# Performance work log

Measured on AMD Instinct MI355X. Metric: run time of the kernel, lower is better.

Reference implementation:

```python
import math
import jax, jax.numpy as jnp
from jax import lax
import numpy as np

B, C, H, W = 2, 48, 64, 64
DI, DS, DCONV, DTR = 96, 16, 4, 3   # d_inner=expand*dim, d_state, d_conv, dt_rank=ceil(48/16)
HF = 96                              # SEFN hidden = dim * ffn_expansion_factor(2)


def _posenc(L, d):
    pos = jnp.arange(L, dtype=jnp.float32)[:, None]
    div = jnp.exp(jnp.arange(0, d, 2, dtype=jnp.float32) * (-math.log(10000.0) / d))
    pe = jnp.zeros((L, d), jnp.float32)
    pe = pe.at[:, 0::2].set(jnp.sin(pos * div))
    pe = pe.at[:, 1::2].set(jnp.cos(pos * div))
    return pe


def _ln(x, w, b, eps=1e-5):  # last-dim LayerNorm, biased variance (torch unbiased=False)
    mu = x.mean(-1, keepdims=True)
    var = ((x - mu) ** 2).mean(-1, keepdims=True)
    return (x - mu) / jnp.sqrt(var + eps) * w + b


def _ln4d(x, w, b):  # WithBias LayerNorm over channel dim of NCHW (to_3d/to_4d round trip)
    b_, c_, h_, w_ = x.shape
    xf = x.reshape(b_, c_, h_ * w_).transpose(0, 2, 1)
    return _ln(xf, w, b).transpose(0, 2, 1).reshape(b_, c_, h_, w_)


def _flip_odd(x):  # flip last axis on odd rows of axis -2 (snake reordering)
    return x.at[:, :, 1::2, :].set(x[:, :, 1::2, ::-1])


def _conv2d(x, w, bias=None, groups=1, pad=0):
    y = lax.conv_general_dilated(x, w, (1, 1), [(pad, pad), (pad, pad)],
                                 feature_group_count=groups,
                                 dimension_numbers=('NCHW', 'OIHW', 'NCHW'))
    if bias is not None:
        y = y + bias[None, :, None, None]
    return y


def _mamba(x, inproj, convw, convb, xproj, dtw, dtb, Alog, D, outproj):
    # standard mamba_ssm Mamba forward; x: (B, L, C)
    b_, L, _ = x.shape
    xz = x @ inproj.T                      # (B, L, 2*DI)
    xm, z = xz[..., :DI], xz[..., DI:]
    xc = xm.transpose(0, 2, 1)             # (B, DI, L)
    xc = lax.conv_general_dilated(xc, convw, (1,), [(DCONV - 1, 0)],
                                  feature_group_count=DI,
                                  dimension_numbers=('NCH', 'OIH', 'NCH'))
    xc = jax.nn.silu(xc + convb[None, :, None]).transpose(0, 2, 1)  # (B, L, DI)
    x_dbl = xc @ xproj.T                   # (B, L, DTR + 2*DS)
    dt = jax.nn.softplus(x_dbl[..., :DTR] @ dtw.T + dtb)            # (B, L, DI)
    Bm = x_dbl[..., DTR:DTR + DS]          # (B, L, DS)
    Cm = x_dbl[..., DTR + DS:]             # (B, L, DS)
    A = -jnp.exp(Alog)                     # (DI, DS)
    dA = jnp.exp(dt[..., None] * A)        # (B, L, DI, DS)
    dBx = dt[..., None] * Bm[:, :, None, :] * xc[..., None]

    def step(h, t):
        dA_t, dBx_t, C_t = t
        h = dA_t * h + dBx_t
        return h, jnp.einsum('bds,bs->bd', h, C_t)

    h0 = jnp.zeros((b_, DI, DS), x.dtype)
    _, ys = lax.scan(step, h0, (dA.transpose(1, 0, 2, 3), dBx.transpose(1, 0, 2, 3), Cm.transpose(1, 0, 2)))
    y = ys.transpose(1, 0, 2) + xc * D
    y = y * jax.nn.silu(z)
    return y @ outproj.T


def _forward(x, n1_w, n1_b, n2_w, n2_b, mln1_w, mln1_b, mln2_w, mln2_b,
             m1, m2, f_pin, f_dw, f_fus, f_dwa, f_pout,
             f_c1w, f_c1b, f_ln1_w, f_ln1_b, f_c2w, f_c2b, f_ln2_w, f_ln2_b):
    x_spatial = x
    L = H * W
    pe = _posenc(L, C)
    # --- MambaLayer: bidirectional flip-scan ---
    xn = _ln4d(x, n1_w, n1_b)
    rev1 = _flip_odd(xn)                               # snake order over rows
    rev2 = _flip_odd(xn.transpose(0, 1, 3, 2))         # snake order over cols
    x1_flat = rev1.reshape(B, C, L).transpose(0, 2, 1) + pe
    x2_flat = rev2.reshape(B, C, L).transpose(0, 2, 1) + pe
    y1 = _mamba(_ln(x1_flat, mln1_w, mln1_b), *m1)
    y2 = _mamba(_ln(x2_flat, mln2_w, mln2_b), *m2)
    out1 = _flip_odd(y1.transpose(0, 2, 1).reshape(B, C, H, W))
    out2 = _flip_odd(y2.transpose(0, 2, 1).reshape(B, C, W, H)).transpose(0, 1, 3, 2)
    x = x + out1 + out2
    # --- SEFN ---
    xn2 = _ln4d(x, n2_w, n2_b)
    xp = _conv2d(xn2, f_pin)                           # (B, 2*HF, H, W)
    y = x_spatial.reshape(B, C, H // 2, 2, W // 2, 2).mean((3, 5))   # AvgPool2d(2)
    y = jax.nn.relu(_ln4d(_conv2d(y, f_c1w, f_c1b, pad=1), f_ln1_w, f_ln1_b))
    y = jax.nn.relu(_ln4d(_conv2d(y, f_c2w, f_c2b, pad=1), f_ln2_w, f_ln2_b))
    y = jnp.repeat(jnp.repeat(y, 2, axis=2), 2, axis=3)              # nearest Upsample(2)
    xd = _conv2d(xp, f_dw, groups=2 * HF, pad=1)
    x1, x2 = xd[:, :HF], xd[:, HF:]
    x1 = _conv2d(jnp.concatenate([x1, y], axis=1), f_fus)
    x1 = _conv2d(x1, f_dwa, groups=HF, pad=1)
    ff = _conv2d(jax.nn.gelu(x1, approximate=False) * x2, f_pout)
    return x + ff


def setup_inputs():
    key = jax.random.key(0)
    ks = iter(jax.random.split(key, 64))

    def nrm(shape, s):
        return s * jax.random.normal(next(ks), shape, jnp.float32)

    inp = {}
    inp['x'] = nrm((B, C, H, W), 1.0)
    for nm in ['n1', 'n2', 'mln1', 'mln2', 'f_ln1', 'f_ln2']:
        inp[nm + '_w'] = jnp.ones((C,), jnp.float32)
        inp[nm + '_b'] = jnp.zeros((C,), jnp.float32)
    for p in ['m1', 'm2']:
        inp[p + '_inproj'] = nrm((2 * DI, C), 0.1)
        inp[p + '_convw'] = nrm((DI, 1, DCONV), 0.3)
        inp[p + '_convb'] = jnp.zeros((DI,), jnp.float32)
        inp[p + '_xproj'] = nrm((DTR + 2 * DS, DI), 0.1)
        inp[p + '_dtw'] = nrm((DI, DTR), 0.3)
        u = jax.random.uniform(next(ks), (DI,), jnp.float32)
        inp[p + '_dtb'] = jnp.log(jnp.expm1(0.001 + 0.099 * u))  # mamba dt bias init
        inp[p + '_Alog'] = jnp.log(jnp.tile(jnp.arange(1., DS + 1., dtype=jnp.float32), (DI, 1)))
        inp[p + '_D'] = jnp.ones((DI,), jnp.float32)
        inp[p + '_outproj'] = nrm((C, DI), 0.1)
    inp['f_pin'] = nrm((2 * HF, C, 1, 1), 0.1)
    inp['f_dw'] = nrm((2 * HF, 1, 3, 3), 0.2)
    inp['f_fus'] = nrm((HF, HF + C, 1, 1), 0.08)
    inp['f_dwa'] = nrm((HF, 1, 3, 3), 0.2)
    inp['f_pout'] = nrm((C, HF, 1, 1), 0.1)
    inp['f_c1w'] = nrm((C, C, 3, 3), 0.05)
    inp['f_c1b'] = jnp.zeros((C,), jnp.float32)
    inp['f_c2w'] = nrm((C, C, 3, 3), 0.05)
    inp['f_c2b'] = jnp.zeros((C,), jnp.float32)
    return inp


def reference(x, n1_w, n1_b, n2_w, n2_b, mln1_w, mln1_b, mln2_w, mln2_b,
              m1_inproj, m1_convw, m1_convb, m1_xproj, m1_dtw, m1_dtb, m1_Alog, m1_D, m1_outproj,
              m2_inproj, m2_convw, m2_convb, m2_xproj, m2_dtw, m2_dtb, m2_Alog, m2_D, m2_outproj,
              f_pin, f_dw, f_fus, f_dwa, f_pout,
              f_c1w, f_c1b, f_ln1_w, f_ln1_b, f_c2w, f_c2b, f_ln2_w, f_ln2_b):
    m1 = (m1_inproj, m1_convw, m1_convb, m1_xproj, m1_dtw, m1_dtb, m1_Alog, m1_D, m1_outproj)
    m2 = (m2_inproj, m2_convw, m2_convb, m2_xproj, m2_dtw, m2_dtb, m2_Alog, m2_D, m2_outproj)
    return _forward(x, n1_w, n1_b, n2_w, n2_b, mln1_w, mln1_b, mln2_w, mln2_b,
                    m1, m2, f_pin, f_dw, f_fus, f_dwa, f_pout,
                    f_c1w, f_c1b, f_ln1_w, f_ln1_b, f_c2w, f_c2b, f_ln2_w, f_ln2_b)
```

## Files before the change

### kernel.cpp

```cpp
#include <hip/hip_runtime.h>

#define DEV __device__ __forceinline__

DEV float siluf(float x){ return x / (1.f + __expf(-x)); }
DEV float softplusf(float x){ return fmaxf(x, 0.f) + log1pf(expf(-fabsf(x))); }
DEV float geluf(float x){ return 0.5f * x * (1.f + erff(x * 0.70710678118654752440f)); }

__global__ __launch_bounds__(256) void kA_front(const float* __restrict__ x,
    const float* __restrict__ n1w, const float* __restrict__ n1b,
    const float* __restrict__ mw0, const float* __restrict__ mb0,
    const float* __restrict__ mw1, const float* __restrict__ mb1,
    const float* __restrict__ ip0, const float* __restrict__ ip1,
    float* __restrict__ xmg, float* __restrict__ Vg){
  __shared__ alignas(16) float Vl[48*36];
  __shared__ float Wt[48*97];
  __shared__ float mu_s[32], rs_s[32];
  int bd = blockIdx.x >> 7, tile = blockIdx.x & 127;
  int dir = bd >> 1, b = bd & 1;
  int t0 = tile*32;
  int tid = threadIdx.x;
  const float* ip = dir ? ip1 : ip0;
  const float* mw = dir ? mw1 : mw0;
  const float* mb = dir ? mb1 : mb0;
  for (int i = tid; i < 96*48; i += 256){
    int j = i / 48, c = i % 48;
    Wt[c*97 + j] = ip[i];
  }
  for (int i = tid; i < 48*32; i += 256){
    int c = i >> 5, r = i & 31;
    int t = t0 + r;
    int h, w;
    if (dir == 0){ h = t >> 6; int wp = t & 63; w = (h & 1) ? 63 - wp : wp; }
    else         { w = t >> 6; int hp = t & 63; h = (w & 1) ? 63 - hp : hp; }
    Vl[c*36 + r] = x[(size_t)b*48*4096 + c*4096 + h*64 + w];
  }
  __syncthreads();
  {
    int r = tid >> 3, k = tid & 7;
    float s1 = 0.f, s2 = 0.f;
    #pragma unroll
    for (int cc = 0; cc < 6; cc++){
      float v = Vl[(k*6+cc)*36 + r];
      s1 += v; s2 += v*v;
    }
    s1 += __shfl_xor(s1,1); s2 += __shfl_xor(s2,1);
    s1 += __shfl_xor(s1,2); s2 += __shfl_xor(s2,2);
    s1 += __shfl_xor(s1,4); s2 += __shfl_xor(s2,4);
    if (k == 0){
      float m = s1*(1.f/48.f);
      mu_s[r] = m;
      rs_s[r] = rsqrtf(s2*(1.f/48.f) - m*m + 1e-5f);
    }
  }
  __syncthreads();
  for (int i = tid; i < 32*48; i += 256){
    int r = i / 48, c = i % 48;
    int t = t0 + r;
    float v = Vl[c*36 + r];
    float xn = (v - mu_s[r])*rs_s[r]*n1w[c] + n1b[c];
    float ang = (float)t * __expf(-(float)(c & ~1) * (9.210340371976184f/48.f));
    float pe = (c & 1) ? cosf(ang) : sinf(ang);
    Vl[c*36 + r] = xn + pe;
  }
  __syncthreads();
  {
    int r = tid >> 3, k = tid & 7;
    float s1 = 0.f, s2 = 0.f;
    #pragma unroll
    for (int cc = 0; cc < 6; cc++){
      float v = Vl[(k*6+cc)*36 + r];
      s1 += v; s2 += v*v;
    }
    s1 += __shfl_xor(s1,1); s2 += __shfl_xor(s2,1);
    s1 += __shfl_xor(s1,2); s2 += __shfl_xor(s2,2);
    s1 += __shfl_xor(s1,4); s2 += __shfl_xor(s2,4);
    if (k == 0){
      float m = s1*(1.f/48.f);
      mu_s[r] = m;
      rs_s[r] = rsqrtf(s2*(1.f/48.f) - m*m + 1e-5f);
    }
  }
  __syncthreads();
  for (int i = tid; i < 32*48; i += 256){
    int r = i / 48, c = i % 48;
    float v = Vl[c*36 + r];
    float v2 = (v - mu_s[r])*rs_s[r]*mw[c] + mb[c];
    Vl[c*36 + r] = v2;
    Vg[((size_t)bd*4096 + t0 + r)*48 + c] = v2;
  }
  __syncthreads();
  for (int k = 0; k < 3; k++){
    int i = tid + k*256;
    int j = i % 96, rb = i / 96;
    float a0=0.f, a1=0.f, a2=0.f, a3=0.f;
    #pragma unroll 4
    for (int c = 0; c < 48; c++){
      float wv = Wt[c*97 + j];
      const float4 v4 = *(const float4*)&Vl[c*36 + rb*4];
      a0 += wv*v4.x; a1 += wv*v4.y; a2 += wv*v4.z; a3 += wv*v4.w;
    }
    size_t g = ((size_t)bd*4096 + t0 + rb*4)*96 + j;
    xmg[g] = a0; xmg[g+96] = a1; xmg[g+192] = a2; xmg[g+288] = a3;
  }
}

__global__ __launch_bounds__(384) void kB_convscan(const float* __restrict__ xmg,
    const float* __restrict__ cwp0, const float* __restrict__ cwp1,
    const float* __restrict__ cbp0, const float* __restrict__ cbp1,
    const float* __restrict__ xpp0, const float* __restrict__ xpp1,
    const float* __restrict__ dwp0, const float* __restrict__ dwp1,
    const float* __restrict__ dbp0, const float* __restrict__ dbp1,
    const float* __restrict__ Alog0, const float* __restrict__ Alog1,
    float* __restrict__ xcg, float* __restrict__ dtg,
    float* __restrict__ Bmg, float* __restrict__ Cmg,
    float* __restrict__ P, float* __restrict__ S){
  __shared__ union UB {
    float xml[96*36];
    struct { float xwl[35*96]; float xdbl[35*33]; } p;
  } ub;
  __shared__ float xcl[96*33];
  __shared__ float dtl[96*33];
  __shared__ alignas(16) float Bl[32*16], Cl[32*16];
  __shared__ float cw[96*4], cbv[96], dwl[96*3], dbl[96];
  int bd = blockIdx.x >> 7, tile = blockIdx.x & 127;
  int dir = bd >> 1;
  int t0 = tile*32;
  int tid = threadIdx.x;
  const float* cwp = dir ? cwp1 : cwp0;
  const float* cbp = dir ? cbp1 : cbp0;
  const float* xpp = dir ? xpp1 : xpp0;
  const float* dwp = dir ? dwp1 : dwp0;
  const float* dbp = dir ? dbp1 : dbp0;
  const float* Alog = dir ? Alog1 : Alog0;
  for (int i = tid; i < 35*96; i += 384){
    int tl = i / 96, d = i % 96;
    int t = t0 - 3 + tl;
    ub.xml[d*36 + tl] = (t >= 0) ? xmg[((size_t)bd*4096 + t)*96 + d] : 0.f;
  }
  for (int i = tid; i < 96*4;  i += 384) cw[i] = cwp[i];
  for (int i = tid; i < 96*3;  i += 384) dwl[i] = dwp[i];
  for (int i = tid; i < 96;    i += 384){ cbv[i] = cbp[i]; dbl[i] = dbp[i]; }
  __syncthreads();
  for (int i = tid; i < 96*32; i += 384){
    int d = i >> 5, t = i & 31;
    float acc = cbv[d];
    #pragma unroll
    for (int k = 0; k < 4; k++) acc += cw[d*4+k]*ub.xml[d*36 + t + k];
    xcl[d*33 + t] = siluf(acc);
  }
  __syncthreads();
  for (int i = tid; i < 35*96; i += 384) ub.p.xwl[i] = xpp[i];
  __syncthreads();
  for (int i = tid; i < 35*32; i += 384){
    int j = i / 32, t = i % 32;
    float acc = 0.f;
    #pragma unroll 4
    for (int d = 0; d < 96; d++) acc += xcl[d*33 + t]*ub.p.xwl[j*96 + d];
    ub.p.xdbl[j*33 + t] = acc;
  }
  __syncthreads();
  for (int i = tid; i < 96*32; i += 384){
    int d = i >> 5, t = i & 31;
    float v = dbl[d];
    #pragma unroll
    for (int r = 0; r < 3; r++) v += ub.p.xdbl[r*33 + t]*dwl[d*3 + r];
    dtl[d*33 + t] = softplusf(v);
  }
  for (int i = tid; i < 32*16; i += 384){
    int t = i / 16, s = i % 16;
    Bl[t*16 + s] = ub.p.xdbl[(3+s)*33 + t];
    Cl[t*16 + s] = ub.p.xdbl[(19+s)*33 + t];
  }
  __syncthreads();
  for (int i = tid; i < 32*96; i += 384){
    int t = i / 96, d = i % 96;
    size_t g = ((size_t)bd*4096 + t0 + t)*96 + d;
    xcg[g] = xcl[d*33 + t];
    dtg[g] = dtl[d*33 + t];
  }
  for (int i = tid; i < 32*16; i += 384){
    int t = i / 16, s = i % 16;
    size_t g = ((size_t)bd*4096 + t0 + t)*16 + s;
    Bmg[g] = Bl[t*16 + s];
    Cmg[g] = Cl[t*16 + s];
  }
  {
    int d = tid >> 2, q = tid & 3;
    float A0 = -__expf(Alog[d*16 + q*4 + 0]);
    float A1 = -__expf(Alog[d*16 + q*4 + 1]);
    float A2 = -__expf(Alog[d*16 + q*4 + 2]);
    float A3 = -__expf(Alog[d*16 + q*4 + 3]);
    float h0=0.f,h1=0.f,h2=0.f,h3=0.f, p0=1.f,p1=1.f,p2=1.f,p3=1.f;
    #pragma unroll 4
    for (int t = 0; t < 32; t++){
      float dtd = dtl[d*33 + t];
      float u = dtd * xcl[d*33 + t];
      const float4 b4 = *(const float4*)&Bl[t*16 + q*4];
      float a0 = __expf(dtd*A0), a1 = __expf(dtd*A1), a2 = __expf(dtd*A2), a3 = __expf(dtd*A3);
      h0 = a0*h0 + u*b4.x; p0 *= a0;
      h1 = a1*h1 + u*b4.y; p1 *= a1;
      h2 = a2*h2 + u*b4.z; p2 *= a2;
      h3 = a3*h3 + u*b4.w; p3 *= a3;
    }
    size_t ob = (size_t)blockIdx.x*1536 + d*16 + q*4;
    *(float4*)&P[ob] = make_float4(p0,p1,p2,p3);
    *(float4*)&S[ob] = make_float4(h0,h1,h2,h3);
  }
}

__global__ __launch_bounds__(256) void k4_comb(float* __restrict__ P, const float* __restrict__ S){
  int tid2 = blockIdx.x*256 + threadIdx.x;
  int bd = tid2 / 1536, r = tid2 % 1536;
  size_t idx = (size_t)bd*128*1536 + r;
  const int ST = 1536;
  float pb0,pb1,pb2,pb3,pb4,pb5,pb6,pb7, sb0,sb1,sb2,sb3,sb4,sb5,sb6,sb7;
  pb0=P[idx+0*ST]; sb0=S[idx+0*ST]; pb1=P[idx+1*ST]; sb1=S[idx+1*ST];
  pb2=P[idx+2*ST]; sb2=S[idx+2*ST]; pb3=P[idx+3*ST]; sb3=S[idx+3*ST];
  pb4=P[idx+4*ST]; sb4=S[idx+4*ST]; pb5=P[idx+5*ST]; sb5=S[idx+5*ST];
  pb6=P[idx+6*ST]; sb6=S[idx+6*ST]; pb7=P[idx+7*ST]; sb7=S[idx+7*ST];
  float h = 0.f;
  for (int c0 = 0; c0 < 128; c0 += 8){
    float pn0=0,sn0=0,pn1=0,sn1=0,pn2=0,sn2=0,pn3=0,sn3=0;
    float pn4=0,sn4=0,pn5=0,sn5=0,pn6=0,sn6=0,pn7=0,sn7=0;
    if (c0 + 8 < 128){
      pn0=P[idx+(size_t)(c0+8)*ST];  sn0=S[idx+(size_t)(c0+8)*ST];
      pn1=P[idx+(size_t)(c0+9)*ST];  sn1=S[idx+(size_t)(c0+9)*ST];
      pn2=P[idx+(size_t)(c0+10)*ST]; sn2=S[idx+(size_t)(c0+10)*ST];
      pn3=P[idx+(size_t)(c0+11)*ST]; sn3=S[idx+(size_t)(c0+11)*ST];
      pn4=P[idx+(size_t)(c0+12)*ST]; sn4=S[idx+(size_t)(c0+12)*ST];
      pn5=P[idx+(size_t)(c0+13)*ST]; sn5=S[idx+(size_t)(c0+13)*ST];
      pn6=P[idx+(size_t)(c0+14)*ST]; sn6=S[idx+(size_t)(c0+14)*ST];
      pn7=P[idx+(size_t)(c0+15)*ST]; sn7=S[idx+(size_t)(c0+15)*ST];
    }
    P[idx+(size_t)(c0+0)*ST] = h; h = pb0*h + sb0;
    P[idx+(size_t)(c0+1)*ST] = h; h = pb1*h + sb1;
    P[idx+(size_t)(c0+2)*ST] = h; h = pb2*h + sb2;
    P[idx+(size_t)(c0+3)*ST] = h; h = pb3*h + sb3;
    P[idx+(size_t)(c0+4)*ST] = h; h = pb4*h + sb4;
    P[idx+(size_t)(c0+5)*ST] = h; h = pb5*h + sb5;
    P[idx+(size_t)(c0+6)*ST] = h; h = pb6*h + sb6;
    P[idx+(size_t)(c0+7)*ST] = h; h = pb7*h + sb7;
    pb0=pn0;sb0=sn0;pb1=pn1;sb1=sn1;pb2=pn2;sb2=sn2;pb3=pn3;sb3=sn3;
    pb4=pn4;sb4=sn4;pb5=pn5;sb5=sn5;pb6=pn6;sb6=sn6;pb7=pn7;sb7=sn7;
  }
}

__global__ __launch_bounds__(384) void k5_scan2(const float* __restrict__ dtg,
    const float* __restrict__ xcg, const float* __restrict__ Bmg, const float* __restrict__ Cmg,
    const float* __restrict__ Alog0, const float* __restrict__ Alog1,
    const float* __restrict__ Dp0, const float* __restrict__ Dp1,
    const float* __restrict__ ip0, const float* __restrict__ ip1,
    const float* __restrict__ Vg, const float* __restrict__ Hin, float* __restrict__ yout){
  __shared__ union U5 {
    struct { float dts[32*96]; float xcs[32*96]; } s;
    struct { float Wzt[48*96]; float Vgs[32*48]; } e;
  } u;
  __shared__ alignas(16) float Bl[32*16], Cl[32*16];
  __shared__ float yl[32*96];
  int task = blockIdx.x;
  int bd = task >> 7, ch = task & 127;
  int t0 = ch*32;
  int tid = threadIdx.x;
  const float* ip   = (bd >= 2) ? ip1 : ip0;
  const float* Alog = (bd >= 2) ? Alog1 : Alog0;
  const float* Dp   = (bd >= 2) ? Dp1 : Dp0;
  for (int i = tid; i < 32*96; i += 384){
    int t = i / 96, dd = i % 96;
    size_t g = ((size_t)bd*4096 + t0 + t)*96 + dd;
    u.s.dts[i] = dtg[g];
    u.s.xcs[i] = xcg[g];
  }
  for (int i = tid; i < 32*16; i += 384){
    size_t g = ((size_t)bd*4096 + t0)*16 + i;
    Bl[i] = Bmg[g];
    Cl[i] = Cmg[g];
  }
  __syncthreads();
  {
    int d = tid >> 2, q = tid & 3;
    float A0 = -__expf(Alog[d*16 + q*4 + 0]);
    float A1 = -__expf(Alog[d*16 + q*4 + 1]);
    float A2 = -__expf(Alog[d*16 + q*4 + 2]);
    float A3 = -__expf(Alog[d*16 + q*4 + 3]);
    float Dd = Dp[d];
    const float4 h4 = *(const float4*)&Hin[(size_t)task*1536 + d*16 + q*4];
    float h0 = h4.x, h1 = h4.y, h2 = h4.z, h3 = h4.w;
    for (int t = 0; t < 32; t += 2){
      float dtdA = u.s.dts[t*96 + d];
      float xcvA = u.s.xcs[t*96 + d];
      float dtdB = u.s.dts[(t+1)*96 + d];
      float xcvB = u.s.xcs[(t+1)*96 + d];
      float uA = dtdA * xcvA, uB = dtdB * xcvB;
      const float4 b4A = *(const float4*)&Bl[t*16 + q*4];
      const float4 c4A = *(const float4*)&Cl[t*16 + q*4];
      const float4 b4B = *(const float4*)&Bl[(t+1)*16 + q*4];
      const float4 c4B = *(const float4*)&Cl[(t+1)*16 + q*4];
      float a0 = __expf(dtdA*A0), a1 = __expf(dtdA*A1), a2 = __expf(dtdA*A2), a3 = __expf(dtdA*A3);
      float e0 = __expf(dtdB*A0), e1 = __expf(dtdB*A1), e2 = __expf(dtdB*A2), e3 = __expf(dtdB*A3);
      h0 = a0*h0 + uA*b4A.x;
      h1 = a1*h1 + uA*b4A.y;
      h2 = a2*h2 + uA*b4A.z;
      h3 = a3*h3 + uA*b4A.w;
      float pyA = (h0*c4A.x + h1*c4A.y) + (h2*c4A.z + h3*c4A.w);
      h0 = e0*h0 + uB*b4B.x;
      h1 = e1*h1 + uB*b4B.y;
      h2 = e2*h2 + uB*b4B.z;
      h3 = e3*h3 + uB*b4B.w;
      float pyB = (h0*c4B.x + h1*c4B.y) + (h2*c4B.z + h3*c4B.w);
      pyA += __shfl_xor(pyA, 1);  pyB += __shfl_xor(pyB, 1);
      pyA += __shfl_xor(pyA, 2);  pyB += __shfl_xor(pyB, 2);
      if (q == 0){
        yl[t*96 + d]     = pyA + xcvA*Dd;
        yl[(t+1)*96 + d] = pyB + xcvB*Dd;
      }
    }
  }
  __syncthreads();
  for (int i = tid; i < 96*48; i += 384){
    int j = i % 96, c = i / 96;
    u.e.Wzt[c*96 + j] = ip[(96 + j)*48 + c];
  }
  for (int i = tid; i < 32*48; i += 384){
    int t = i / 48, c = i % 48;
    u.e.Vgs[i] = Vg[((size_t)bd*4096 + t0 + t)*48 + c];
  }
  __syncthreads();
  for (int i = tid; i < 32*96; i += 384){
    int t = i / 96, dd = i % 96;
    float z = 0.f;
    #pragma unroll 4
    for (int c = 0; c < 48; c++) z += u.e.Wzt[c*96 + dd] * u.e.Vgs[t*48 + c];
    size_t g = ((size_t)bd*4096 + t0 + t)*96 + dd;
    yout[g] = yl[i] * siluf(z);
  }
}

__global__ __launch_bounds__(384) void k67_mid(const float* __restrict__ x,
    const float* __restrict__ y1, const float* __restrict__ y2,
    const float* __restrict__ op1, const float* __restrict__ op2,
    const float* __restrict__ nw, const float* __restrict__ nb,
    const float* __restrict__ pin,
    float* __restrict__ xmid, float* __restrict__ xp){
  __shared__ float bufW[192*49];
  __shared__ union UL { float ylds[16*97]; struct { float xl[48*17]; float mu[16]; float rs[16]; } l; } ul;
  int bid = blockIdx.x;
  int b = bid >> 8, h = (bid >> 2) & 63, wq = bid & 3;
  int w0 = wq << 4;
  int tid = threadIdx.x;
  int w = tid & 15, cg = tid >> 4;
  float acc0 = 0.f, acc1 = 0.f;
  for (int pass = 0; pass < 2; pass++){
    __syncthreads();
    const float* op = pass ? op2 : op1;
    const float* y  = pass ? y2  : y1;
    for (int i = tid; i < 48*96; i += 384){
      int c = i / 96, d = i % 96;
      bufW[c*97 + d] = op[i];
    }
    if (pass == 0){
      for (int i = tid; i < 16*96; i += 384){
        int wl_ = i / 96, d = i % 96;
        int wsp = w0 + wl_;
        int wp = (h & 1) ? 63 - wsp : wsp;
        ul.ylds[wl_*97 + d] = y[((size_t)b*4096 + h*64 + wp)*96 + d];
      }
    } else {
      for (int i = tid; i < 16*96; i += 384){
        int wl_ = i / 96, d = i % 96;
        int wsp = w0 + wl_;
        int t = wsp*64 + ((wsp & 1) ? 63 - h : h);
        ul.ylds[wl_*97 + d] = y[((size_t)b*4096 + t)*96 + d];
      }
    }
    __syncthreads();
    #pragma unroll 4
    for (int d = 0; d < 96; d++){
      float yv = ul.ylds[w*97 + d];
      acc0 += yv * bufW[(cg*2+0)*97 + d];
      acc1 += yv * bufW[(cg*2+1)*97 + d];
    }
  }
  __syncthreads();
  {
    int c0 = cg*2;
    size_t idx0 = (((size_t)b*48 + c0)*64 + h)*64 + w0 + w;
    float v0 = x[idx0] + acc0;
    xmid[idx0] = v0;
    ul.l.xl[c0*17 + w] = v0;
    size_t idx1 = idx0 + 4096;
    float v1 = x[idx1] + acc1;
    xmid[idx1] = v1;
    ul.l.xl[(c0+1)*17 + w] = v1;
  }
  for (int i = tid; i < 192*48; i += 384){
    int r = i / 48, c = i % 48;
    bufW[r*49 + c] = pin[i];
  }
  __syncthreads();
  if (tid < 128){
    int r = tid >> 3, k = tid & 7;
    float s1 = 0.f, s2 = 0.f;
    #pragma unroll
    for (int cc = 0; cc < 6; cc++){
      float v = ul.l.xl[(k*6+cc)*17 + r];
      s1 += v; s2 += v*v;
    }
    s1 += __shfl_xor(s1,1); s2 += __shfl_xor(s2,1);
    s1 += __shfl_xor(s1,2); s2 += __shfl_xor(s2,2);
    s1 += __shfl_xor(s1,4); s2 += __shfl_xor(s2,4);
    if (k == 0){
      float m = s1*(1.f/48.f);
      ul.l.mu[r] = m;
      ul.l.rs[r] = rsqrtf(s2*(1.f/48.f) - m*m + 1e-5f);
    }
  }
  __syncthreads();
  for (int i = tid; i < 48*16; i += 384){
    int c = i >> 4, ww = i & 15;
    ul.l.xl[c*17 + ww] = (ul.l.xl[c*17 + ww] - ul.l.mu[ww])*ul.l.rs[ww]*nw[c] + nb[c];
  }
  __syncthreads();
  for (int it = 0; it < 2; it++){
    int i = tid + it*384;
    int ww = i & 15, oq = i >> 4;
    int o0 = oq*4;
    float a0=0,a1=0,a2=0,a3=0;
    #pragma unroll 4
    for (int c = 0; c < 48; c++){
      float xv = ul.l.xl[c*17 + ww];
      a0 += xv*bufW[(o0+0)*49 + c];
      a1 += xv*bufW[(o0+1)*49 + c];
      a2 += xv*bufW[(o0+2)*49 + c];
      a3 += xv*bufW[(o0+3)*49 + c];
    }
    xp[(((size_t)b*192 + o0+0)*64 + h)*64 + w0 + ww] = a0;
    xp[(((size_t)b*192 + o0+1)*64 + h)*64 + w0 + ww] = a1;
    xp[(((size_t)b*192 + o0+2)*64 + h)*64 + w0 + ww] = a2;
    xp[(((size_t)b*192 + o0+3)*64 + h)*64 + w0 + ww] = a3;
  }
}

__global__ __launch_bounds__(384) void k9_conv3(const float* __restrict__ in,
    const float* __restrict__ wgt, const float* __restrict__ bias,
    const float* __restrict__ lnw, const float* __restrict__ lnb,
    float* __restrict__ out, int pooled, int lnin){
  __shared__ float wl[12*48*9];
  __shared__ float sin_[48*3*34];
  __shared__ float mu_i[104], rs_i[104];
  int bid = blockIdx.x;
  int cq = bid & 3, i0 = (bid >> 2) & 31, b = bid >> 7;
  int tid = threadIdx.x;
  for (int i = tid; i < 12*48*9; i += 384) wl[i] = wgt[cq*12*48*9 + i];
  for (int i = tid; i < 48*3*34; i += 384){
    int jx = i % 34, ky = (i/34) % 3, ci = i/102;
    int r = i0 + ky - 1, j = jx - 1;
    float v = 0.f;
    if (r >= 0 && r < 32 && j >= 0 && j < 32){
      if (pooled){
        const float* xb = in + (((size_t)b*48 + ci)*64 + 2*r)*64 + 2*j;
        v = 0.25f*(xb[0] + xb[1] + xb[64] + xb[65]);
      } else {
        v = in[(((size_t)b*48 + ci)*32 + r)*32 + j];
      }
    }
    sin_[i] = v;
  }
  __syncthreads();
  if (lnin){
    if (tid < 102){
      int jx = tid % 34, ky = tid / 34;
      int r = i0 + ky - 1, j = jx - 1;
      if (r >= 0 && r < 32 && j >= 0 && j < 32){
        float s1 = 0.f, s2 = 0.f;
        #pragma unroll 4
        for (int ci = 0; ci < 48; ci++){ float v = sin_[ci*102 + tid]; s1 += v; s2 += v*v; }
        float m = s1*(1.f/48.f);
        mu_i[tid] = m;
        rs_i[tid] = rsqrtf(s2*(1.f/48.f) - m*m + 1e-5f);
      }
    }
    __syncthreads();
    for (int i = tid; i < 48*102; i += 384){
      int ci = i / 102, p = i % 102;
      int jx = p % 34, ky = p / 34;
      int r = i0 + ky - 1, j = jx - 1;
      if (r >= 0 && r < 32 && j >= 0 && j < 32){
        float v = (sin_[i] - mu_i[p])*rs_i[p]*lnw[ci] + lnb[ci];
        sin_[i] = fmaxf(v, 0.f);
      }
    }
    __syncthreads();
  }
  int j = tid & 31, col = tid >> 5;
  float acc = bias[cq*12 + col];
  for (int ci = 0; ci < 48; ci++){
    const float* wp = wl + ((size_t)col*48 + ci)*9;
    const float* sp = sin_ + ci*102;
    #pragma unroll
    for (int ky = 0; ky < 3; ky++)
      #pragma unroll
      for (int kx = 0; kx < 3; kx++)
        acc += sp[ky*34 + j + kx] * wp[ky*3 + kx];
  }
  out[(((size_t)b*48 + cq*12 + col)*32 + i0)*32 + j] = acc;
}

__global__ __launch_bounds__(256) void k13_dw(const float* __restrict__ in,
    const float* __restrict__ wgt, float* __restrict__ out, int CH){
  int idx = blockIdx.x*256 + threadIdx.x;
  if (idx >= 2*CH*1024) return;
  int wq = idx & 15, h = (idx >> 4) & 63, c = (idx >> 10) % CH, b = idx / (CH*1024);
  int w0 = wq*4;
  const float* ip = in + ((size_t)b*CH + c)*4096;
  const float* wp = wgt + c*9;
  float a0=0.f,a1=0.f,a2=0.f,a3=0.f;
  #pragma unroll
  for (int ky = 0; ky < 3; ky++){
    int hh = h + ky - 1;
    if (hh < 0 || hh > 63) continue;
    const float* rp = ip + hh*64;
    float v0 = (w0 > 0)  ? rp[w0-1] : 0.f;
    float v1 = rp[w0+0], v2 = rp[w0+1], v3 = rp[w0+2], v4 = rp[w0+3];
    float v5 = (w0 < 60) ? rp[w0+4] : 0.f;
    float k0 = wp[ky*3+0], k1 = wp[ky*3+1], k2 = wp[ky*3+2];
    a0 += k0*v0 + k1*v1 + k2*v2;
    a1 += k0*v1 + k1*v2 + k2*v3;
    a2 += k0*v2 + k1*v3 + k2*v4;
    a3 += k0*v3 + k1*v4 + k2*v5;
  }
  float* op = out + (((size_t)b*CH + c)*64 + h)*64 + w0;
  op[0]=a0; op[1]=a1; op[2]=a2; op[3]=a3;
}

__global__ __launch_bounds__(256) void k14_fus(const float* __restrict__ xd,
    const float* __restrict__ cv2, const float* __restrict__ lnw, const float* __restrict__ lnb,
    const float* __restrict__ fus, float* __restrict__ x1){
  __shared__ float wl[48*144];
  __shared__ float al[96][64];
  __shared__ float yl[48][32];
  __shared__ float muy[32], rsy[32];
  int bid = blockIdx.x;
  int oh = bid & 1, h = (bid >> 1) & 63, b = bid >> 7;
  int tid = threadIdx.x;
  for (int i = tid; i < 48*144; i += 256) wl[i] = fus[(size_t)oh*48*144 + i];
  for (int i = tid; i < 96*64; i += 256){
    int ci = i >> 6, w = i & 63;
    al[ci][w] = xd[(((size_t)b*192 + ci)*64 + h)*64 + w];
  }
  for (int i = tid; i < 48*32; i += 256){
    int cj = i >> 5, j = i & 31;
    yl[cj][j] = cv2[(((size_t)b*48 + cj)*32 + (h >> 1))*32 + j];
  }
  __syncthreads();
  if (tid < 32){
    float s1 = 0.f, s2 = 0.f;
    #pragma unroll 4
    for (int cj = 0; cj < 48; cj++){ float v = yl[cj][tid]; s1 += v; s2 += v*v; }
    float m = s1*(1.f/48.f);
    muy[tid] = m;
    rsy[tid] = rsqrtf(s2*(1.f/48.f) - m*m + 1e-5f);
  }
  __syncthreads();
  for (int i = tid; i < 48*32; i += 256){
    int cj = i >> 5, j = i & 31;
    yl[cj][j] = fmaxf((yl[cj][j] - muy[j])*rsy[j]*lnw[cj] + lnb[cj], 0.f);
  }
  __syncthreads();
  for (int it = 0; it < 3; it++){
    int i = tid + it*256;
    int w = i & 63, ob = i >> 6; int o0 = ob*4;
    float a[4] = {0,0,0,0};
    #pragma unroll 4
    for (int ci = 0; ci < 96; ci++){
      float xv = al[ci][w];
      #pragma unroll
      for (int q = 0; q < 4; q++) a[q] += xv * wl[(o0+q)*144 + ci];
    }
    int w2 = w >> 1;
    #pragma unroll 4
    for (int cj = 0; cj < 48; cj++){
      float yv = yl[cj][w2];
      #pragma unroll
      for (int q = 0; q < 4; q++) a[q] += yv * wl[(o0+q)*144 + 96 + cj];
    }
    #pragma unroll
    for (int q = 0; q < 4; q++)
      x1[(((size_t)b*96 + oh*48 + o0 + q)*64 + h)*64 + w] = a[q];
  }
}

__global__ __launch_bounds__(384) void k16_out(const float* __restrict__ x1,
    const float* __restrict__ xd, const float* __restrict__ dww,
    const float* __restrict__ pout, const float* __restrict__ xmid, float* __restrict__ out){
  __shared__ float wl[48*97];
  __shared__ float xs[96*54];
  __shared__ float gl[96*17];
  __shared__ float dwl[96*9];
  int bid = blockIdx.x;
  int b = bid >> 8, h = (bid >> 2) & 63, wq = bid & 3;
  int w0 = wq << 4;
  int tid = threadIdx.x;
  for (int i = tid; i < 48*96; i += 384){
    int r = i / 96, c = i % 96;
    wl[r*97 + c] = pout[i];
  }
  for (int i = tid; i < 96*9; i += 384) dwl[i] = dww[i];
  for (int i = tid; i < 96*54; i += 384){
    int jx = i % 18, ky = (i/18) % 3, ch = i/54;
    int hh = h + ky - 1, ww_ = w0 + jx - 1;
    float v = 0.f;
    if (hh >= 0 && hh < 64 && ww_ >= 0 && ww_ < 64)
      v = x1[(((size_t)b*96 + ch)*64 + hh)*64 + ww_];
    xs[i] = v;
  }
  __syncthreads();
  for (int i = tid; i < 96*16; i += 384){
    int ch = i >> 4, ww = i & 15;
    const float* wp = dwl + ch*9;
    const float* sp = xs + ch*54;
    float a = 0.f;
    #pragma unroll
    for (int ky = 0; ky < 3; ky++)
      #pragma unroll
      for (int kx = 0; kx < 3; kx++)
        a += sp[ky*18 + ww + kx] * wp[ky*3 + kx];
    float x2 = xd[(((size_t)b*192 + 96 + ch)*64 + h)*64 + w0 + ww];
    gl[ch*17 + ww] = geluf(a) * x2;
  }
  __syncthreads();
  int ww = tid & 15, cg = tid >> 4;
  float a0=0.f, a1=0.f;
  #pragma unroll 4
  for (int ch = 0; ch < 96; ch++){
    float gv = gl[ch*17 + ww];
    a0 += gv * wl[(cg*2+0)*97 + ch];
    a1 += gv * wl[(cg*2+1)*97 + ch];
  }
  {
    int c0 = cg*2;
    size_t idx0 = (((size_t)b*48 + c0)*64 + h)*64 + w0 + ww;
    out[idx0] = xmid[idx0] + a0;
    size_t idx1 = idx0 + 4096;
    out[idx1] = xmid[idx1] + a1;
  }
}

extern "C" void kernel_launch(void* const* d_in, const int* in_sizes, int n_in,
                              void* d_out, int out_size, void* d_ws, size_t ws_size,
                              hipStream_t stream){
  (void)in_sizes; (void)n_in; (void)out_size; (void)ws_size;
  const float* x    = (const float*)d_in[0];
  const float* n1w  = (const float*)d_in[1];
  const float* n1b  = (const float*)d_in[2];
  const float* n2w  = (const float*)d_in[3];
  const float* n2b  = (const float*)d_in[4];
  const float* mlnw[2] = {(const float*)d_in[5], (const float*)d_in[7]};
  const float* mlnb[2] = {(const float*)d_in[6], (const float*)d_in[8]};
  const float* fln1w = (const float*)d_in[9];
  const float* fln1b = (const float*)d_in[10];
  const float* fln2w = (const float*)d_in[11];
  const float* fln2b = (const float*)d_in[12];
  const float* inproj[2]  = {(const float*)d_in[13], (const float*)d_in[22]};
  const float* convw[2]   = {(const float*)d_in[14], (const float*)d_in[23]};
  const float* convb[2]   = {(const float*)d_in[15], (const float*)d_in[24]};
  const float* xproj[2]   = {(const float*)d_in[16], (const float*)d_in[25]};
  const float* dtw[2]     = {(const float*)d_in[17], (const float*)d_in[26]};
  const float* dtbp[2]    = {(const float*)d_in[18], (const float*)d_in[27]};
  const float* Alog[2]    = {(const float*)d_in[19], (const float*)d_in[28]};
  const float* Dp[2]      = {(const float*)d_in[20], (const float*)d_in[29]};
  const float* outproj[2] = {(const float*)d_in[21], (const float*)d_in[30]};
  const float* fpin  = (const float*)d_in[31];
  const float* fdw   = (const float*)d_in[32];
  const float* ffus  = (const float*)d_in[33];
  const float* fdwa  = (const float*)d_in[34];
  const float* fpout = (const float*)d_in[35];
  const float* fc1w  = (const float*)d_in[36];
  const float* fc1b  = (const float*)d_in[37];
  const float* fc2w  = (const float*)d_in[38];
  const float* fc2b  = (const float*)d_in[39];

  float* ws = (float*)d_ws;
  float* xmg = ws + 0;
  float* Vgb = ws + 1572864;
  float* xcg = ws + 2359296;
  float* dtg = ws + 3932160;
  float* Bmg = ws + 5505024;
  float* Cmg = ws + 5767168;
  float* Pb  = ws + 6029312;
  float* Sb  = ws + 6815744;
  float* xmid= ws + 7602176;
  float* yall = xmg;
  float* Hin  = Pb;
  float* ta   = Sb;
  float* tbuf = Sb + 98304;
  float* xpb  = xcg;
  float* xdb  = dtg;
  float* x1b  = Pb;

  kA_front<<<512,256,0,stream>>>(x, n1w, n1b,
      mlnw[0], mlnb[0], mlnw[1], mlnb[1], inproj[0], inproj[1], xmg, Vgb);
  kB_convscan<<<512,384,0,stream>>>(xmg,
      convw[0], convw[1], convb[0], convb[1], xproj[0], xproj[1],
      dtw[0], dtw[1], dtbp[0], dtbp[1], Alog[0], Alog[1],
      xcg, dtg, Bmg, Cmg, Pb, Sb);
  k4_comb  <<<24,256,0,stream>>>(Pb, Sb);
  k5_scan2 <<<512,384,0,stream>>>(dtg, xcg, Bmg, Cmg, Alog[0], Alog[1],
      Dp[0], Dp[1], inproj[0], inproj[1], Vgb, Hin, yall);
  k67_mid  <<<512,384,0,stream>>>(x, yall, yall + 786432, outproj[0], outproj[1],
      n2w, n2b, fpin, xmid, xpb);
  k9_conv3 <<<256,384,0,stream>>>(x,  fc1w, fc1b, fln1w, fln1b, ta,   1, 0);
  k9_conv3 <<<256,384,0,stream>>>(ta, fc2w, fc2b, fln1w, fln1b, tbuf, 0, 1);
  k13_dw   <<<1536,256,0,stream>>>(xpb, fdw, xdb, 192);
  k14_fus  <<<256,256,0,stream>>>(xdb, tbuf, fln2w, fln2b, ffus, x1b);
  k16_out  <<<512,384,0,stream>>>(x1b, xdb, fdwa, fpout, xmid, (float*)d_out);
}
```

Measured before the change: 184.8 us.

## Fuse depthwise 3x3 conv into fusion and output kernels, drop k13_dw

Removes the standalone depthwise conv kernel over 192 channels. The first 96 channels are now convolved inside k14_fus from a halo tile of xp, with k14_fus retiled to 16-wide column chunks over 1024 blocks. The second 96 channels are recomputed inside k16_out alongside the existing depthwise conv. This eliminates one launch and the write and read of the intermediate xd buffer, at the cost of redundant halo loads, extra shared memory, and a reworked 1x1 matmul tiling in k14.

```diff
diff --git a/kernel.cpp b/kernel.cpp
--- a/kernel.cpp
+++ b/kernel.cpp
@@ -505,97 +505,87 @@
   out[(((size_t)b*48 + cq*12 + col)*32 + i0)*32 + j] = acc;
 }
 
-__global__ __launch_bounds__(256) void k13_dw(const float* __restrict__ in,
-    const float* __restrict__ wgt, float* __restrict__ out, int CH){
-  int idx = blockIdx.x*256 + threadIdx.x;
-  if (idx >= 2*CH*1024) return;
-  int wq = idx & 15, h = (idx >> 4) & 63, c = (idx >> 10) % CH, b = idx / (CH*1024);
-  int w0 = wq*4;
-  const float* ip = in + ((size_t)b*CH + c)*4096;
-  const float* wp = wgt + c*9;
-  float a0=0.f,a1=0.f,a2=0.f,a3=0.f;
-  #pragma unroll
-  for (int ky = 0; ky < 3; ky++){
-    int hh = h + ky - 1;
-    if (hh < 0 || hh > 63) continue;
-    const float* rp = ip + hh*64;
-    float v0 = (w0 > 0)  ? rp[w0-1] : 0.f;
-    float v1 = rp[w0+0], v2 = rp[w0+1], v3 = rp[w0+2], v4 = rp[w0+3];
-    float v5 = (w0 < 60) ? rp[w0+4] : 0.f;
-    float k0 = wp[ky*3+0], k1 = wp[ky*3+1], k2 = wp[ky*3+2];
-    a0 += k0*v0 + k1*v1 + k2*v2;
-    a1 += k0*v1 + k1*v2 + k2*v3;
-    a2 += k0*v2 + k1*v3 + k2*v4;
-    a3 += k0*v3 + k1*v4 + k2*v5;
-  }
-  float* op = out + (((size_t)b*CH + c)*64 + h)*64 + w0;
-  op[0]=a0; op[1]=a1; op[2]=a2; op[3]=a3;
-}
-
-__global__ __launch_bounds__(256) void k14_fus(const float* __restrict__ xd,
+__global__ __launch_bounds__(256) void k14_fus(const float* __restrict__ xp,
     const float* __restrict__ cv2, const float* __restrict__ lnw, const float* __restrict__ lnb,
-    const float* __restrict__ fus, float* __restrict__ x1){
-  __shared__ float wl[48*144];
-  __shared__ float al[96][64];
-  __shared__ float yl[48][32];
-  __shared__ float muy[32], rsy[32];
+    const float* __restrict__ dww, const float* __restrict__ fus, float* __restrict__ x1){
+  __shared__ float wl[48*145];
+  __shared__ float xps[96*54];
+  __shared__ float dwl[96*9];
+  __shared__ float ylq[48*9];
+  __shared__ float gl[96*17];
+  __shared__ float muy[8], rsy[8];
   int bid = blockIdx.x;
-  int oh = bid & 1, h = (bid >> 1) & 63, b = bid >> 7;
+  int wq = bid & 3, h = (bid >> 2) & 63, oh = (bid >> 8) & 1, b = bid >> 9;
+  int w0 = wq << 4;
   int tid = threadIdx.x;
-  for (int i = tid; i < 48*144; i += 256) wl[i] = fus[(size_t)oh*48*144 + i];
-  for (int i = tid; i < 96*64; i += 256){
-    int ci = i >> 6, w = i & 63;
-    al[ci][w] = xd[(((size_t)b*192 + ci)*64 + h)*64 + w];
-  }
-  for (int i = tid; i < 48*32; i += 256){
-    int cj = i >> 5, j = i & 31;
-    yl[cj][j] = cv2[(((size_t)b*48 + cj)*32 + (h >> 1))*32 + j];
-  }
-  __syncthreads();
-  if (tid < 32){
+  for (int i = tid; i < 48*144; i += 256){
+    int r = i / 144, c = i % 144;
+    wl[r*145 + c] = fus[(size_t)oh*48*144 + i];
+  }
+  for (int i = tid; i < 96*9; i += 256) dwl[i] = dww[i];
+  for (int i = tid; i < 96*54; i += 256){
+    int jx = i % 18, ky = (i/18) % 3, ci = i/54;
+    int hh = h + ky - 1, ww_ = w0 + jx - 1;
+    float v = 0.f;
+    if (hh >= 0 && hh < 64 && ww_ >= 0 && ww_ < 64)
+      v = xp[(((size_t)b*192 + ci)*64 + hh)*64 + ww_];
+    xps[i] = v;
+  }
+  {
+    int hp = h >> 1, j0 = w0 >> 1;
+    for (int i = tid; i < 48*8; i += 256){
+      int cj = i >> 3, jl = i & 7;
+      ylq[cj*9 + jl] = cv2[(((size_t)b*48 + cj)*32 + hp)*32 + j0 + jl];
+    }
+  }
+  __syncthreads();
+  if (tid < 8){
     float s1 = 0.f, s2 = 0.f;
     #pragma unroll 4
-    for (int cj = 0; cj < 48; cj++){ float v = yl[cj][tid]; s1 += v; s2 += v*v; }
+    for (int cj = 0; cj < 48; cj++){ float v = ylq[cj*9 + tid]; s1 += v; s2 += v*v; }
     float m = s1*(1.f/48.f);
     muy[tid] = m;
     rsy[tid] = rsqrtf(s2*(1.f/48.f) - m*m + 1e-5f);
   }
-  __syncthreads();
-  for (int i = tid; i < 48*32; i += 256){
-    int cj = i >> 5, j = i & 31;
-    yl[cj][j] = fmaxf((yl[cj][j] - muy[j])*rsy[j]*lnw[cj] + lnb[cj], 0.f);
+  for (int i = tid; i < 96*16; i += 256){
+    int ci = i >> 4, ww = i & 15;
+    const float* wp = dwl + ci*9;
+    const float* sp = xps + ci*54;
+    float a = 0.f;
+    #pragma unroll
+    for (int ky = 0; ky < 3; ky++)
+      #pragma unroll
+      for (int kx = 0; kx < 3; kx++)
+        a += sp[ky*18 + ww + kx] * wp[ky*3 + kx];
+    gl[ci*17 + ww] = a;
+  }
+  __syncthreads();
+  for (int i = tid; i < 48*8; i += 256){
+    int cj = i >> 3, jl = i & 7;
+    ylq[cj*9 + jl] = fmaxf((ylq[cj*9 + jl] - muy[jl])*rsy[jl]*lnw[cj] + lnb[cj], 0.f);
   }
   __syncthreads();
   for (int it = 0; it < 3; it++){
     int i = tid + it*256;
-    int w = i & 63, ob = i >> 6; int o0 = ob*4;
-    float a[4] = {0,0,0,0};
-    #pragma unroll 4
-    for (int ci = 0; ci < 96; ci++){
-      float xv = al[ci][w];
-      #pragma unroll
-      for (int q = 0; q < 4; q++) a[q] += xv * wl[(o0+q)*144 + ci];
-    }
-    int w2 = w >> 1;
-    #pragma unroll 4
-    for (int cj = 0; cj < 48; cj++){
-      float yv = yl[cj][w2];
-      #pragma unroll
-      for (int q = 0; q < 4; q++) a[q] += yv * wl[(o0+q)*144 + 96 + cj];
-    }
-    #pragma unroll
-    for (int q = 0; q < 4; q++)
-      x1[(((size_t)b*96 + oh*48 + o0 + q)*64 + h)*64 + w] = a[q];
+    int ww = i & 15, o = i >> 4;
+    float a = 0.f;
+    #pragma unroll 4
+    for (int ci = 0; ci < 96; ci++) a += gl[ci*17 + ww] * wl[o*145 + ci];
+    int jl = ww >> 1;
+    #pragma unroll 4
+    for (int cj = 0; cj < 48; cj++) a += ylq[cj*9 + jl] * wl[o*145 + 96 + cj];
+    x1[(((size_t)b*96 + oh*48 + o)*64 + h)*64 + w0 + ww] = a;
   }
 }
 
 __global__ __launch_bounds__(384) void k16_out(const float* __restrict__ x1,
-    const float* __restrict__ xd, const float* __restrict__ dww,
+    const float* __restrict__ xp, const float* __restrict__ dwa, const float* __restrict__ dwf2,
     const float* __restrict__ pout, const float* __restrict__ xmid, float* __restrict__ out){
   __shared__ float wl[48*97];
   __shared__ float xs[96*54];
+  __shared__ float xs2[96*54];
   __shared__ float gl[96*17];
-  __shared__ float dwl[96*9];
+  __shared__ float dwl[96*9], dwl2[96*9];
   int bid = blockIdx.x;
   int b = bid >> 8, h = (bid >> 2) & 63, wq = bid & 3;
   int w0 = wq << 4;
@@ -604,27 +594,33 @@
     int r = i / 96, c = i % 96;
     wl[r*97 + c] = pout[i];
   }
-  for (int i = tid; i < 96*9; i += 384) dwl[i] = dww[i];
+  for (int i = tid; i < 96*9; i += 384){ dwl[i] = dwa[i]; dwl2[i] = dwf2[i]; }
   for (int i = tid; i < 96*54; i += 384){
     int jx = i % 18, ky = (i/18) % 3, ch = i/54;
     int hh = h + ky - 1, ww_ = w0 + jx - 1;
-    float v = 0.f;
-    if (hh >= 0 && hh < 64 && ww_ >= 0 && ww_ < 64)
-      v = x1[(((size_t)b*96 + ch)*64 + hh)*64 + ww_];
-    xs[i] = v;
+    float v1 = 0.f, v2 = 0.f;
+    if (hh >= 0 && hh < 64 && ww_ >= 0 && ww_ < 64){
+      v1 = x1[(((size_t)b*96 + ch)*64 + hh)*64 + ww_];
+      v2 = xp[(((size_t)b*192 + 96 + ch)*64 + hh)*64 + ww_];
+    }
+    xs[i] = v1;
+    xs2[i] = v2;
   }
   __syncthreads();
   for (int i = tid; i < 96*16; i += 384){
     int ch = i >> 4, ww = i & 15;
     const float* wp = dwl + ch*9;
     const float* sp = xs + ch*54;
-    float a = 0.f;
+    const float* wp2 = dwl2 + ch*9;
+    const float* sp2 = xs2 + ch*54;
+    float a = 0.f, x2 = 0.f;
     #pragma unroll
     for (int ky = 0; ky < 3; ky++)
       #pragma unroll
-      for (int kx = 0; kx < 3; kx++)
-        a += sp[ky*18 + ww + kx] * wp[ky*3 + kx];
-    float x2 = xd[(((size_t)b*192 + 96 + ch)*64 + h)*64 + w0 + ww];
+      for (int kx = 0; kx < 3; kx++){
+        a  += sp [ky*18 + ww + kx] * wp [ky*3 + kx];
+        x2 += sp2[ky*18 + ww + kx] * wp2[ky*3 + kx];
+      }
     gl[ch*17 + ww] = geluf(a) * x2;
   }
   __syncthreads();
@@ -694,7 +690,6 @@
   float* ta   = Sb;
   float* tbuf = Sb + 98304;
   float* xpb  = xcg;
-  float* xdb  = dtg;
   float* x1b  = Pb;
 
   kA_front<<<512,256,0,stream>>>(x, n1w, n1b,
@@ -710,7 +705,6 @@
       n2w, n2b, fpin, xmid, xpb);
   k9_conv3 <<<256,384,0,stream>>>(x,  fc1w, fc1b, fln1w, fln1b, ta,   1, 0);
   k9_conv3 <<<256,384,0,stream>>>(ta, fc2w, fc2b, fln1w, fln1b, tbuf, 0, 1);
-  k13_dw   <<<1536,256,0,stream>>>(xpb, fdw, xdb, 192);
-  k14_fus  <<<256,256,0,stream>>>(xdb, tbuf, fln2w, fln2b, ffus, x1b);
-  k16_out  <<<512,384,0,stream>>>(x1b, xdb, fdwa, fpout, xmid, (float*)d_out);
-}
+  k14_fus  <<<1024,256,0,stream>>>(xpb, tbuf, fln2w, fln2b, fdw, ffus, x1b);
+  k16_out  <<<512,384,0,stream>>>(x1b, xpb, fdwa, fdw + 96*9, fpout, xmid, (float*)d_out);
+}
```

After: 208.9 us. 1.13x slower.
